# Kernel tuning notes

Hardware: AMD Instinct MI355X
Metric: run time of the kernel (lower is better)

Reference implementation:

```python
import jax, jax.numpy as jnp
import numpy as np

L, C, H, DH, M, NP, HID, NCLS, EPS = 12, 768, 12, 64, 64, 197, 3072, 1000, 1e-6

def layer_norm(x, w, b):
    mu = x.mean(-1, keepdims=True)
    var = ((x - mu) ** 2).mean(-1, keepdims=True)
    return (x - mu) * jax.lax.rsqrt(var + EPS) * w + b

def softmax_kernel(data, w, is_query):
    # data: (B,N,H,dh), w: (m,dh). Faithful to source: projection uses raw data
    # (no normalizer), and diag term is sum(data)/2 * d^{-1/2} (as written).
    d = data.shape[-1]
    dn = 1.0 / np.sqrt(np.sqrt(d))
    ratio = 1.0 / np.sqrt(np.sqrt(M))
    dd = jnp.einsum('blhd,md->blhm', data, w)
    diag = (data.sum(-1) / 2.0) * dn * dn  # (B,N,H)
    diag = diag[..., None]
    if is_query:
        stab = jnp.max(dd, axis=-1, keepdims=True)
    else:
        stab = jnp.max(dd)
    return ratio * (jnp.exp(dd - diag - stab) + 1e-6)

def performer_attn(x, qkv_w, qkv_b, w_orf, proj_w, proj_b):
    B, N, _ = x.shape
    qkv = (x @ qkv_w.T + qkv_b).reshape(B, N, 3, H, DH)
    q, k, v = qkv[:, :, 0], qkv[:, :, 1], qkv[:, :, 2]  # (B,N,H,dh)
    kp = softmax_kernel(k, w_orf, False)
    qp = softmax_kernel(q, w_orf, True)
    kv = jnp.einsum('blhm,blhd->bhmd', kp, v)
    num = jnp.einsum('blhm,bhmd->blhd', qp, kv)
    ks = kp.sum(1)  # (B,H,m)
    D = jnp.einsum('blhm,bhm->blh', qp, ks)[..., None]
    out = (num / D).reshape(B, N, C)
    return out @ proj_w.T + proj_b

def setup_inputs() -> dict:
    rng = np.random.default_rng(0)
    def rn(*s, scale=0.02):
        return jnp.asarray(rng.standard_normal(s, dtype=np.float32) * scale)
    # Gaussian orthogonal random features per layer (m == head_dim -> one QR block)
    w_orf = []
    for _ in range(L):
        blk = rng.standard_normal((DH, DH)).astype(np.float32)
        q, _ = np.linalg.qr(blk)
        mult = np.linalg.norm(rng.standard_normal((M, DH)).astype(np.float32), axis=1)
        w_orf.append(np.diag(mult) @ q.T)
    inp = {
        'x': jnp.asarray(rng.standard_normal((32, 3, 224, 224), dtype=np.float32)),
        'patch_w': rn(C, 3, 16, 16), 'patch_b': rn(C),
        'cls_token': rn(1, 1, C), 'pos_embed': rn(1, NP, C),
        'ln1_w': jnp.ones((L, C), jnp.float32), 'ln1_b': jnp.zeros((L, C), jnp.float32),
        'qkv_w': rn(L, 3 * C, C), 'qkv_b': jnp.zeros((L, 3 * C), jnp.float32),
        'w_orf': jnp.asarray(np.stack(w_orf)),
        'proj_w': rn(L, C, C), 'proj_b': jnp.zeros((L, C), jnp.float32),
        'ln2_w': jnp.ones((L, C), jnp.float32), 'ln2_b': jnp.zeros((L, C), jnp.float32),
        'fc1_w': rn(L, HID, C), 'fc1_b': jnp.zeros((L, HID), jnp.float32),
        'fc2_w': rn(L, C, HID), 'fc2_b': jnp.zeros((L, C), jnp.float32),
        'lnf_w': jnp.ones((C,), jnp.float32), 'lnf_b': jnp.zeros((C,), jnp.float32),
        'head_w': rn(NCLS, C), 'head_b': jnp.zeros((NCLS,), jnp.float32),
    }
    return inp

def reference(x, patch_w, patch_b, cls_token, pos_embed, ln1_w, ln1_b, qkv_w, qkv_b,
              w_orf, proj_w, proj_b, ln2_w, ln2_b, fc1_w, fc1_b, fc2_w, fc2_b,
              lnf_w, lnf_b, head_w, head_b):
    B = x.shape[0]
    # patch embed: 16x16 stride-16 conv -> (B, 196, 768)
    t = jax.lax.conv_general_dilated(x, patch_w, (16, 16), 'VALID',
                                     dimension_numbers=('NCHW', 'OIHW', 'NCHW'))
    t = t.reshape(B, C, -1).transpose(0, 2, 1) + patch_b
    t = jnp.concatenate([jnp.broadcast_to(cls_token, (B, 1, C)), t], axis=1) + pos_embed
    for i in range(L):
        t = t + performer_attn(layer_norm(t, ln1_w[i], ln1_b[i]),
                               qkv_w[i], qkv_b[i], w_orf[i], proj_w[i], proj_b[i])
        h = layer_norm(t, ln2_w[i], ln2_b[i])
        h = jax.nn.gelu(h @ fc1_w[i].T + fc1_b[i], approximate=False)
        t = t + (h @ fc2_w[i].T + fc2_b[i])
    t = layer_norm(t, lnf_w, lnf_b)
    return t[:, 0] @ head_w.T + head_b
```

## Files before the change

kernel.cpp:

```cpp
#include <hip/hip_runtime.h>
#include <hip/hip_bf16.h>
#include <math.h>

typedef __hip_bfloat16 bf16;

#define B_    32
#define L_    12
#define C_    768
#define H_    12
#define DH_   64
#define M_    64
#define NP_   197
#define HID_  3072
#define NCLS_ 1000
#define NTOK   (B_*NP_)
#define NPATCH (B_*196)

typedef unsigned long long u64;

__device__ __forceinline__ float ldin(const void* p, int isb, u64 i){
  return isb ? __bfloat162float(((const bf16*)p)[i]) : ((const float*)p)[i];
}

__device__ __forceinline__ unsigned short f2b(float f){
  unsigned u = __float_as_uint(f);
  u += 0x7FFFu + ((u >> 16) & 1u);
  return (unsigned short)(u >> 16);
}

__device__ __forceinline__ unsigned fkey(float f){
  unsigned u = __float_as_uint(f);
  return (u & 0x80000000u) ? ~u : (u | 0x80000000u);
}
__device__ __forceinline__ float kfloat(unsigned k){
  return __uint_as_float((k & 0x80000000u) ? (k ^ 0x80000000u) : ~k);
}

__global__ void k_detect(const void* ln1w, int* flag){
  if (threadIdx.x==0 && blockIdx.x==0)
    *flag = (((const unsigned*)ln1w)[0] == 0x3F800000u) ? 0 : 1;
}

__global__ void k_init(unsigned* Smax){
  if (threadIdx.x < L_) Smax[threadIdx.x] = 0u;
}

__global__ void k_im2col(const void* __restrict__ x, float* __restrict__ P,
                         const int* __restrict__ flag){
  int isb = *flag;
  int idx = blockIdx.x*256 + threadIdx.x;
  if (idx >= NPATCH*768) return;
  int row = idx / 768, col = idx - row*768;
  int b = row / 196, p = row - b*196;
  int py = p / 14, px = p - py*14;
  int i = col >> 8, r = col & 255, ky = r >> 4, kx = r & 15;
  P[idx] = ldin(x, isb, ((u64)(b*3+i)*224 + py*16+ky)*224 + px*16 + kx);
}

__global__ void k_assemble(const float* __restrict__ PG, const void* __restrict__ patch_b,
                           const void* __restrict__ cls, const void* __restrict__ pos,
                           float* __restrict__ T, const int* __restrict__ flag){
  int isb = *flag;
  int idx = blockIdx.x*256 + threadIdx.x;
  if (idx >= NTOK*C_) return;
  int c = idx % C_; int t = idx / C_; int n = t % NP_; int b = t / NP_;
  float v;
  if (n == 0) v = ldin(cls, isb, c) + ldin(pos, isb, c);
  else v = PG[(u64)(b*196 + n-1)*C_ + c] + ldin(patch_b, isb, c)
         + ldin(pos, isb, (u64)n*C_ + c);
  T[idx] = v;
}

__global__ void k_ln(const float* __restrict__ X, const void* __restrict__ w,
                     const void* __restrict__ bb, float* __restrict__ Y, int rowStride,
                     const int* __restrict__ flag, u64 wOff){
  int isb = *flag;
  int r = blockIdx.x;
  const float* xr = X + (u64)r*rowStride*C_;
  float* yr = Y + (u64)r*C_;
  int tid = threadIdx.x;
  int lane = tid & 63, wv = tid >> 6;
  __shared__ float red[8];
  float v[3]; float s = 0.f;
  #pragma unroll
  for (int j=0;j<3;j++){ v[j] = xr[tid + j*256]; s += v[j]; }
  #pragma unroll
  for (int off=32; off; off>>=1) s += __shfl_xor(s, off);
  if (lane==0) red[wv] = s;
  __syncthreads();
  float mu = (red[0]+red[1]+red[2]+red[3]) * (1.0f/768.0f);
  float s2 = 0.f;
  #pragma unroll
  for (int j=0;j<3;j++){ float d = v[j]-mu; s2 += d*d; }
  #pragma unroll
  for (int off=32; off; off>>=1) s2 += __shfl_xor(s2, off);
  if (lane==0) red[4+wv] = s2;
  __syncthreads();
  float rs = rsqrtf((red[4]+red[5]+red[6]+red[7])*(1.0f/768.0f) + 1e-6f);
  #pragma unroll
  for (int j=0;j<3;j++){ int c = tid + j*256;
    yr[c] = (v[j]-mu)*rs*ldin(w,isb,wOff+c) + ldin(bb,isb,wOff+c); }
}

enum {EPI_STORE=0, EPI_GELU=1, EPI_RES=2, EPI_OUT=3};

typedef __attribute__((ext_vector_type(8))) __bf16 bf16x8;
typedef __attribute__((ext_vector_type(4))) float  f32x4;

#define LDP 40

__global__ __launch_bounds__(256, 2) void k_gemm(const float* __restrict__ A,
        const void* __restrict__ W, const void* __restrict__ bias,
        float* __restrict__ D, void* __restrict__ Oany, const int* __restrict__ flag,
        int Rows, int N, int K, int epi, u64 wOff, u64 bOff){
  const int isb = *flag;
  __shared__ __bf16 Ah[128][LDP];
  __shared__ __bf16 Al[128][LDP];
  __shared__ __bf16 Bs[128][LDP];
  const int tid = threadIdx.x;
  const int rb = blockIdx.y*128, cb = blockIdx.x*128;
  const int lane = tid & 63, wv = tid >> 6;
  const int wr = (wv >> 1)*64, wc = (wv & 1)*64;
  const int lr = lane & 15, kb = (lane >> 4)*8;
  const int er = tid >> 2, kq = (tid & 3)*8;
  f32x4 acc[4][4] = {};

  for (int k0 = 0; k0 < K; k0 += 32){
    #pragma unroll
    for (int p = 0; p < 2; ++p){
      int r = er + p*64;
      int row = rb + r;
      float fv[8];
      if (row < Rows){
        const float* ap = A + (u64)row*K + k0 + kq;
        float4 f0 = *(const float4*)ap;
        float4 f1 = *(const float4*)(ap+4);
        fv[0]=f0.x; fv[1]=f0.y; fv[2]=f0.z; fv[3]=f0.w;
        fv[4]=f1.x; fv[5]=f1.y; fv[6]=f1.z; fv[7]=f1.w;
      } else {
        #pragma unroll
        for (int j=0;j<8;j++) fv[j] = 0.f;
      }
      union { uint4 v; unsigned short s[8]; } hi, lo;
      #pragma unroll
      for (int j=0;j<8;j++){
        unsigned short h = f2b(fv[j]);
        hi.s[j] = h;
        float fh = __uint_as_float((unsigned)h << 16);
        lo.s[j] = f2b(fv[j] - fh);
      }
      *(uint4*)&Ah[r][kq] = hi.v;
      *(uint4*)&Al[r][kq] = lo.v;
    }
    #pragma unroll
    for (int p = 0; p < 2; ++p){
      int r = er + p*64;
      int col = cb + r;
      union { uint4 v; unsigned short s[8]; } bw;
      if (col < N){
        if (isb){
          bw.v = *(const uint4*)((const unsigned short*)W + wOff + (u64)col*K + k0 + kq);
        } else {
          const float* wp = (const float*)W + wOff + (u64)col*K + k0 + kq;
          float4 f0 = *(const float4*)wp;
          float4 f1 = *(const float4*)(wp+4);
          bw.s[0]=f2b(f0.x); bw.s[1]=f2b(f0.y); bw.s[2]=f2b(f0.z); bw.s[3]=f2b(f0.w);
          bw.s[4]=f2b(f1.x); bw.s[5]=f2b(f1.y); bw.s[6]=f2b(f1.z); bw.s[7]=f2b(f1.w);
        }
      } else {
        bw.v = make_uint4(0u,0u,0u,0u);
      }
      *(uint4*)&Bs[r][kq] = bw.v;
    }
    __syncthreads();
    bf16x8 ah[4], al[4], bv[4];
    #pragma unroll
    for (int m=0;m<4;m++){
      ah[m] = *(const bf16x8*)&Ah[wr + m*16 + lr][kb];
      al[m] = *(const bf16x8*)&Al[wr + m*16 + lr][kb];
    }
    #pragma unroll
    for (int n=0;n<4;n++) bv[n] = *(const bf16x8*)&Bs[wc + n*16 + lr][kb];
    #pragma unroll
    for (int m=0;m<4;m++)
      #pragma unroll
      for (int n=0;n<4;n++){
        acc[m][n] = __builtin_amdgcn_mfma_f32_16x16x32_bf16(ah[m], bv[n], acc[m][n], 0, 0, 0);
        acc[m][n] = __builtin_amdgcn_mfma_f32_16x16x32_bf16(al[m], bv[n], acc[m][n], 0, 0, 0);
      }
    __syncthreads();
  }

  const int r0 = (lane >> 4)*4;
  #pragma unroll
  for (int m=0;m<4;m++){
    int rowb = rb + wr + m*16 + r0;
    #pragma unroll
    for (int n=0;n<4;n++){
      int col = cb + wc + n*16 + lr;
      if (col >= N) continue;
      float bvv = bias ? ldin(bias, isb, bOff + col) : 0.f;
      #pragma unroll
      for (int r=0;r<4;r++){
        int row = rowb + r;
        if (row >= Rows) continue;
        float v = acc[m][n][r] + bvv;
        u64 off = (u64)row*N + col;
        if (epi == EPI_STORE)      D[off] = v;
        else if (epi == EPI_GELU)  D[off] = 0.5f*v*(1.0f + erff(v*0.70710678118654752f));
        else if (epi == EPI_RES)   D[off] += v;
        else {
          if (isb) ((bf16*)Oany)[off] = __float2bfloat16(v);
          else     ((float*)Oany)[off] = v;
        }
      }
    }
  }
}

__global__ __launch_bounds__(256) void k_phi(const float* __restrict__ QKV,
        const void* __restrict__ worf, float* __restrict__ QP, float* __restrict__ KP,
        unsigned* __restrict__ Smax, const int* __restrict__ flag, u64 wOff){
  const int isb = *flag;
  __shared__ float wT[64][65];
  for (int e = threadIdx.x; e < 4096; e += 256){
    int m = e >> 6, d = e & 63;
    wT[d][m] = ldin(worf, isb, wOff + e);
  }
  __syncthreads();
  const int lane = threadIdx.x & 63, wv = threadIdx.x >> 6;
  const int NRID = NTOK*H_;
  float wmax = -1e30f;
  for (int rid = blockIdx.x*4 + wv; rid < NRID; rid += gridDim.x*4){
    int h = rid % 12, bl = rid / 12;
    const float* base = QKV + (u64)bl*2304 + h*64;
    float qd = base[lane];
    float kd = base[768 + lane];
    float sq = qd, sk = kd;
    #pragma unroll
    for (int off=32; off; off>>=1){ sq += __shfl_xor(sq,off); sk += __shfl_xor(sk,off); }
    float ddq = 0.f, ddk = 0.f;
    #pragma unroll
    for (int d=0; d<64; d++){
      float w = wT[d][lane];
      ddq += __shfl(qd, d)*w;
      ddk += __shfl(kd, d)*w;
    }
    float mq = ddq, mk = ddk;
    #pragma unroll
    for (int off=32; off; off>>=1){
      mq = fmaxf(mq, __shfl_xor(mq,off));
      mk = fmaxf(mk, __shfl_xor(mk,off));
    }
    QP[(u64)rid*64 + lane] = 0.35355339059327f*(expf(ddq - sq*0.0625f - mq) + 1e-6f);
    KP[(u64)rid*64 + lane] = ddk - sk*0.0625f;
    wmax = fmaxf(wmax, mk);
  }
  if (lane == 0) atomicMax(Smax, fkey(wmax));
}

__global__ __launch_bounds__(256) void k_kv(const float* __restrict__ KP,
        const float* __restrict__ QKV, const unsigned* __restrict__ Smax,
        float* __restrict__ KV, float* __restrict__ KS){
  const int bh = blockIdx.x, b = bh/12, h = bh - (bh/12)*12;
  const float S = kfloat(*Smax);
  __shared__ float KPs[16][64];
  __shared__ float Vs[16][64];
  const int t = threadIdx.x;
  const int d = t & 63, mg = t >> 6;
  const int lr = t >> 4, c4 = (t & 15)*4;
  float acc[16] = {};
  float ksacc = 0.f;
  for (int l0 = 0; l0 < NP_; l0 += 16){
    int l = l0 + lr;
    float4 kpv = make_float4(0.f,0.f,0.f,0.f), vv = make_float4(0.f,0.f,0.f,0.f);
    if (l < NP_){
      u64 bl = (u64)(b*NP_ + l);
      float4 r = *(const float4*)(KP + (bl*12 + h)*64 + c4);
      kpv.x = 0.35355339059327f*(expf(r.x - S) + 1e-6f);
      kpv.y = 0.35355339059327f*(expf(r.y - S) + 1e-6f);
      kpv.z = 0.35355339059327f*(expf(r.z - S) + 1e-6f);
      kpv.w = 0.35355339059327f*(expf(r.w - S) + 1e-6f);
      vv = *(const float4*)(QKV + bl*2304 + 1536 + h*64 + c4);
    }
    __syncthreads();
    *(float4*)&KPs[lr][c4] = kpv;
    *(float4*)&Vs[lr][c4]  = vv;
    __syncthreads();
    #pragma unroll
    for (int lc=0; lc<16; lc++){
      float vd = Vs[lc][d];
      #pragma unroll
      for (int j=0;j<16;j++) acc[j] += KPs[lc][mg*16+j]*vd;
    }
    if (t < 64){
      #pragma unroll
      for (int lc=0; lc<16; lc++) ksacc += KPs[lc][t];
    }
  }
  float* kvb = KV + (u64)bh*4096;
  #pragma unroll
  for (int j=0;j<16;j++) kvb[(u64)(mg*16+j)*64 + d] = acc[j];
  if (t < 64) KS[(u64)bh*64 + t] = ksacc;
}

__global__ __launch_bounds__(256) void k_numd(const float* __restrict__ QP,
        const float* __restrict__ KV, const float* __restrict__ KS,
        float* __restrict__ OUT){
  const int bh = blockIdx.x, b = bh/12, h = bh - (bh/12)*12;
  __shared__ float kvs[64][64];
  __shared__ float kss[64];
  const int t = threadIdx.x;
  for (int e = t*4; e < 4096; e += 1024)
    *(float4*)&kvs[0][e] = *(const float4*)(KV + (u64)bh*4096 + e);
  if (t < 64) kss[t] = KS[(u64)bh*64 + t];
  __syncthreads();
  const int lane = t & 63, wv = t >> 6;
  for (int l = wv; l < NP_; l += 4){
    u64 rid = (u64)(b*NP_ + l)*12 + h;
    float q = QP[rid*64 + lane];
    float dp = q*kss[lane];
    #pragma unroll
    for (int off=32; off; off>>=1) dp += __shfl_xor(dp, off);
    float acc = 0.f;
    #pragma unroll
    for (int m=0;m<64;m++) acc += __shfl(q, m)*kvs[m][lane];
    OUT[(u64)(b*NP_ + l)*768 + h*64 + lane] = acc/dp;
  }
}

extern "C" void kernel_launch(void* const* d_in, const int* in_sizes, int n_in,
                              void* d_out, int out_size, void* d_ws, size_t ws_size,
                              hipStream_t stream) {
  const void* x        = d_in[0];
  const void* patch_w  = d_in[1];
  const void* patch_b  = d_in[2];
  const void* cls_tok  = d_in[3];
  const void* pos_emb  = d_in[4];
  const void* ln1_w    = d_in[5];
  const void* ln1_b    = d_in[6];
  const void* qkv_w    = d_in[7];
  const void* qkv_b    = d_in[8];
  const void* w_orf    = d_in[9];
  const void* proj_w   = d_in[10];
  const void* proj_b   = d_in[11];
  const void* ln2_w    = d_in[12];
  const void* ln2_b    = d_in[13];
  const void* fc1_w    = d_in[14];
  const void* fc1_b    = d_in[15];
  const void* fc2_w    = d_in[16];
  const void* fc2_b    = d_in[17];
  const void* lnf_w    = d_in[18];
  const void* lnf_b    = d_in[19];
  const void* head_w   = d_in[20];
  const void* head_b   = d_in[21];

  float* ws = (float*)d_ws;
  const u64 SZ_TOKC = (u64)NTOK*C_;
  const u64 SZ_BIG  = (u64)NTOK*HID_;
  const u64 SZ_PHI  = (u64)NTOK*H_*M_;
  const u64 SZ_KV   = (u64)B_*H_*M_*DH_;
  const u64 SZ_KS   = (u64)B_*H_*M_;
  const u64 SZ_RMX  = (u64)NTOK*H_;

  float* T   = ws;
  float* LNB = T   + SZ_TOKC;
  float* BIG = LNB + SZ_TOKC;
  float* QP  = BIG + SZ_BIG;
  float* KP  = QP  + SZ_PHI;
  float* KV  = KP  + SZ_PHI;
  float* KS  = KV  + SZ_KV;
  float* RMX = KS  + SZ_KS;
  float* SS  = RMX + SZ_RMX;
  unsigned* SMAX = (unsigned*)SS;
  int*   FLG = (int*)(SS + 16);
  float* CLS = SS  + 32;

  k_detect<<<1, 64, 0, stream>>>(ln1_w, FLG);
  k_init<<<1, 64, 0, stream>>>(SMAX);

  k_im2col<<<(NPATCH*768+255)/256, 256, 0, stream>>>(x, BIG, FLG);
  k_gemm<<<dim3(6,49), 256, 0, stream>>>(BIG, patch_w, nullptr, LNB, nullptr, FLG,
                                         NPATCH, 768, 768, EPI_STORE, 0, 0);
  k_assemble<<<(NTOK*C_+255)/256, 256, 0, stream>>>(LNB, patch_b, cls_tok, pos_emb, T, FLG);

  for (int i = 0; i < L_; i++){
    u64 oQW = (u64)i*2304*C_, oQB = (u64)i*2304;
    u64 oPW = (u64)i*C_*C_,   oPB = (u64)i*C_;
    u64 o1W = (u64)i*HID_*C_, o1B = (u64)i*HID_;
    u64 o2W = (u64)i*C_*HID_, o2B = (u64)i*C_;
    u64 oL  = (u64)i*C_;
    u64 oRF = (u64)i*M_*DH_;
    k_ln<<<NTOK, 256, 0, stream>>>(T, ln1_w, ln1_b, LNB, 1, FLG, oL);
    k_gemm<<<dim3(18,50), 256, 0, stream>>>(LNB, qkv_w, qkv_b, BIG, nullptr, FLG,
                                            NTOK, 2304, 768, EPI_STORE, oQW, oQB);
    k_phi<<<512, 256, 0, stream>>>(BIG, w_orf, QP, KP, SMAX+i, FLG, oRF);
    k_kv<<<B_*H_, 256, 0, stream>>>(KP, BIG, SMAX+i, KV, KS);
    k_numd<<<B_*H_, 256, 0, stream>>>(QP, KV, KS, LNB);
    k_gemm<<<dim3(6,50), 256, 0, stream>>>(LNB, proj_w, proj_b, T, nullptr, FLG,
                                           NTOK, 768, 768, EPI_RES, oPW, oPB);
    k_ln<<<NTOK, 256, 0, stream>>>(T, ln2_w, ln2_b, LNB, 1, FLG, oL);
    k_gemm<<<dim3(24,50), 256, 0, stream>>>(LNB, fc1_w, fc1_b, BIG, nullptr, FLG,
                                            NTOK, 3072, 768, EPI_GELU, o1W, o1B);
    k_gemm<<<dim3(6,50), 256, 0, stream>>>(BIG, fc2_w, fc2_b, T, nullptr, FLG,
                                           NTOK, 768, 3072, EPI_RES, o2W, o2B);
  }

  k_ln<<<B_, 256, 0, stream>>>(T, lnf_w, lnf_b, CLS, NP_, FLG, 0);
  k_gemm<<<dim3(8,1), 256, 0, stream>>>(CLS, head_w, head_b, nullptr, d_out, FLG,
                                        B_, NCLS_, 768, EPI_OUT, 0, 0);
}
```

Baseline: 11.45 ms.

## Pre-split activations into bf16 hi/lo and stream GEMM tiles via global_load_lds

Producers (im2col, layernorm, attention output, GELU epilogue) now write activations as separate bf16 high and low halves instead of fp32. The GEMM then loads A and B tiles directly into XOR-swizzled LDS with global_load_lds, using a K step of 64. Work-groups are remapped for XCD-aware, row-stripe locality, and occupancy is raised to 3 blocks per CU. This removes per-tile fp32 to bf16 splitting and the register round-trip. In exchange, rows past the end can be read out of bounds when Rows is not a multiple of 128 (the A loads are unclamped), and the workspace layout is reshuffled.

```diff
diff --git a/kernel.cpp b/kernel.cpp
--- a/kernel.cpp
+++ b/kernel.cpp
@@ -27,6 +27,9 @@
   u += 0x7FFFu + ((u >> 16) & 1u);
   return (unsigned short)(u >> 16);
 }
+__device__ __forceinline__ float b2f(unsigned short h){
+  return __uint_as_float((unsigned)h << 16);
+}
 
 __device__ __forceinline__ unsigned fkey(float f){
   unsigned u = __float_as_uint(f);
@@ -36,6 +39,12 @@
   return __uint_as_float((k & 0x80000000u) ? (k ^ 0x80000000u) : ~k);
 }
 
+__device__ __forceinline__ void gl_lds16(const void* g, void* s){
+  __builtin_amdgcn_global_load_lds((const __attribute__((address_space(1))) unsigned int*)g,
+                                   (__attribute__((address_space(3))) unsigned int*)s,
+                                   16, 0, 0);
+}
+
 __global__ void k_detect(const void* ln1w, int* flag){
   if (threadIdx.x==0 && blockIdx.x==0)
     *flag = (((const unsigned*)ln1w)[0] == 0x3F800000u) ? 0 : 1;
@@ -45,8 +54,8 @@
   if (threadIdx.x < L_) Smax[threadIdx.x] = 0u;
 }
 
-__global__ void k_im2col(const void* __restrict__ x, float* __restrict__ P,
-                         const int* __restrict__ flag){
+__global__ void k_im2col(const void* __restrict__ x, unsigned short* __restrict__ PH,
+                         unsigned short* __restrict__ PL, const int* __restrict__ flag){
   int isb = *flag;
   int idx = blockIdx.x*256 + threadIdx.x;
   if (idx >= NPATCH*768) return;
@@ -54,7 +63,9 @@
   int b = row / 196, p = row - b*196;
   int py = p / 14, px = p - py*14;
   int i = col >> 8, r = col & 255, ky = r >> 4, kx = r & 15;
-  P[idx] = ldin(x, isb, ((u64)(b*3+i)*224 + py*16+ky)*224 + px*16 + kx);
+  float v = ldin(x, isb, ((u64)(b*3+i)*224 + py*16+ky)*224 + px*16 + kx);
+  unsigned short h = f2b(v);
+  PH[idx] = h; PL[idx] = f2b(v - b2f(h));
 }
 
 __global__ void k_assemble(const float* __restrict__ PG, const void* __restrict__ patch_b,
@@ -72,12 +83,12 @@
 }
 
 __global__ void k_ln(const float* __restrict__ X, const void* __restrict__ w,
-                     const void* __restrict__ bb, float* __restrict__ Y, int rowStride,
+                     const void* __restrict__ bb, unsigned short* __restrict__ YH,
+                     unsigned short* __restrict__ YL, int rowStride,
                      const int* __restrict__ flag, u64 wOff){
   int isb = *flag;
   int r = blockIdx.x;
   const float* xr = X + (u64)r*rowStride*C_;
-  float* yr = Y + (u64)r*C_;
   int tid = threadIdx.x;
   int lane = tid & 63, wv = tid >> 6;
   __shared__ float red[8];
@@ -99,7 +110,11 @@
   float rs = rsqrtf((red[4]+red[5]+red[6]+red[7])*(1.0f/768.0f) + 1e-6f);
   #pragma unroll
   for (int j=0;j<3;j++){ int c = tid + j*256;
-    yr[c] = (v[j]-mu)*rs*ldin(w,isb,wOff+c) + ldin(bb,isb,wOff+c); }
+    float o = (v[j]-mu)*rs*ldin(w,isb,wOff+c) + ldin(bb,isb,wOff+c);
+    unsigned short h = f2b(o);
+    YH[(u64)r*C_ + c] = h;
+    YL[(u64)r*C_ + c] = f2b(o - b2f(h));
+  }
 }
 
 enum {EPI_STORE=0, EPI_GELU=1, EPI_RES=2, EPI_OUT=3};
@@ -107,87 +122,100 @@
 typedef __attribute__((ext_vector_type(8))) __bf16 bf16x8;
 typedef __attribute__((ext_vector_type(4))) float  f32x4;
 
-#define LDP 40
-
-__global__ __launch_bounds__(256, 2) void k_gemm(const float* __restrict__ A,
+__global__ __launch_bounds__(256, 3) void k_gemm(
+        const unsigned short* __restrict__ AHp, const unsigned short* __restrict__ ALp,
         const void* __restrict__ W, const void* __restrict__ bias,
-        float* __restrict__ D, void* __restrict__ Oany, const int* __restrict__ flag,
+        float* __restrict__ Df, unsigned short* __restrict__ GH, unsigned short* __restrict__ GL,
+        void* __restrict__ Oany, const int* __restrict__ flag,
         int Rows, int N, int K, int epi, u64 wOff, u64 bOff){
   const int isb = *flag;
-  __shared__ __bf16 Ah[128][LDP];
-  __shared__ __bf16 Al[128][LDP];
-  __shared__ __bf16 Bs[128][LDP];
+  __shared__ __bf16 sAh[128*64];
+  __shared__ __bf16 sAl[128*64];
+  __shared__ __bf16 sBs[128*64];
   const int tid = threadIdx.x;
-  const int rb = blockIdx.y*128, cb = blockIdx.x*128;
   const int lane = tid & 63, wv = tid >> 6;
+
+  const int nx = (N + 127) >> 7;
+  const int nwg = gridDim.x;
+  const int q = nwg >> 3, r8 = nwg & 7;
+  const int xcd = blockIdx.x & 7, sidx = blockIdx.x >> 3;
+  const int wg = (xcd < r8 ? xcd*(q+1) : r8*(q+1) + (xcd-r8)*q) + sidx;
+  const int stripe = wg / (nx*8);
+  const int within = wg - stripe*(nx*8);
+  const int bx = within >> 3, by = stripe*8 + (within & 7);
+  const int rb = by*128, cb = bx*128;
+  if (rb >= Rows) return;
+
   const int wr = (wv >> 1)*64, wc = (wv & 1)*64;
-  const int lr = lane & 15, kb = (lane >> 4)*8;
-  const int er = tid >> 2, kq = (tid & 3)*8;
+  const int lr = lane & 15;
+  const int srow = lane >> 3;
+  const int sgb  = ((lane & 7) ^ srow) * 16;
+  const int wvBase = wv * 32;
+
+  const char* Ahb = (const char*)AHp;
+  const char* Alb = (const char*)ALp;
+  const char* Wb = nullptr; const float* Wf = nullptr;
+  unsigned limB = 0;
+  if (isb){ Wb = (const char*)W + wOff*2; limB = (unsigned)((u64)N*(u64)K*2 - 16); }
+  else      Wf = (const float*)W + wOff;
+
   f32x4 acc[4][4] = {};
 
-  for (int k0 = 0; k0 < K; k0 += 32){
-    #pragma unroll
-    for (int p = 0; p < 2; ++p){
-      int r = er + p*64;
-      int row = rb + r;
-      float fv[8];
-      if (row < Rows){
-        const float* ap = A + (u64)row*K + k0 + kq;
-        float4 f0 = *(const float4*)ap;
-        float4 f1 = *(const float4*)(ap+4);
-        fv[0]=f0.x; fv[1]=f0.y; fv[2]=f0.z; fv[3]=f0.w;
-        fv[4]=f1.x; fv[5]=f1.y; fv[6]=f1.z; fv[7]=f1.w;
-      } else {
+  for (int k0 = 0; k0 < K; k0 += 64){
+    #pragma unroll
+    for (int c = 0; c < 4; ++c){
+      int row = wvBase + c*8 + srow;
+      unsigned aoff = (unsigned)((rb + row)*K + k0)*2u + sgb;
+      gl_lds16(Ahb + aoff, &sAh[(wvBase + c*8)*64]);
+      gl_lds16(Alb + aoff, &sAl[(wvBase + c*8)*64]);
+    }
+    if (isb){
+      #pragma unroll
+      for (int c = 0; c < 4; ++c){
+        int row = wvBase + c*8 + srow;
+        unsigned boff = (unsigned)((cb + row)*K + k0)*2u + sgb;
+        boff = boff < limB ? boff : limB;
+        gl_lds16(Wb + boff, &sBs[(wvBase + c*8)*64]);
+      }
+    } else {
+      for (int e = tid; e < 1024; e += 256){
+        int rr = e >> 3, lg = e & 7;
+        int col = cb + rr;
+        union { uint4 v; unsigned short s[8]; } bw;
+        if (col < N){
+          const float* wp = Wf + (u64)col*K + k0 + lg*8;
+          #pragma unroll
+          for (int j=0;j<8;j++) bw.s[j] = f2b(wp[j]);
+        } else bw.v = make_uint4(0u,0u,0u,0u);
+        *(uint4*)&sBs[rr*64 + (lg ^ (rr & 7))*8] = bw.v;
+      }
+    }
+    __syncthreads();
+    #pragma unroll
+    for (int ks = 0; ks < 2; ++ks){
+      const int g = ks*4 + (lane >> 4);
+      bf16x8 ah[4], al[4], bv[4];
+      #pragma unroll
+      for (int m=0;m<4;m++){
+        int R = wr + m*16 + lr;
+        int gp = (g ^ (R & 7)) * 8;
+        ah[m] = *(const bf16x8*)&sAh[R*64 + gp];
+        al[m] = *(const bf16x8*)&sAl[R*64 + gp];
+      }
+      #pragma unroll
+      for (int n=0;n<4;n++){
+        int R = wc + n*16 + lr;
+        int gp = (g ^ (R & 7)) * 8;
+        bv[n] = *(const bf16x8*)&sBs[R*64 + gp];
+      }
+      #pragma unroll
+      for (int m=0;m<4;m++)
         #pragma unroll
-        for (int j=0;j<8;j++) fv[j] = 0.f;
-      }
-      union { uint4 v; unsigned short s[8]; } hi, lo;
-      #pragma unroll
-      for (int j=0;j<8;j++){
-        unsigned short h = f2b(fv[j]);
-        hi.s[j] = h;
-        float fh = __uint_as_float((unsigned)h << 16);
-        lo.s[j] = f2b(fv[j] - fh);
-      }
-      *(uint4*)&Ah[r][kq] = hi.v;
-      *(uint4*)&Al[r][kq] = lo.v;
-    }
-    #pragma unroll
-    for (int p = 0; p < 2; ++p){
-      int r = er + p*64;
-      int col = cb + r;
-      union { uint4 v; unsigned short s[8]; } bw;
-      if (col < N){
-        if (isb){
-          bw.v = *(const uint4*)((const unsigned short*)W + wOff + (u64)col*K + k0 + kq);
-        } else {
-          const float* wp = (const float*)W + wOff + (u64)col*K + k0 + kq;
-          float4 f0 = *(const float4*)wp;
-          float4 f1 = *(const float4*)(wp+4);
-          bw.s[0]=f2b(f0.x); bw.s[1]=f2b(f0.y); bw.s[2]=f2b(f0.z); bw.s[3]=f2b(f0.w);
-          bw.s[4]=f2b(f1.x); bw.s[5]=f2b(f1.y); bw.s[6]=f2b(f1.z); bw.s[7]=f2b(f1.w);
+        for (int n=0;n<4;n++){
+          acc[m][n] = __builtin_amdgcn_mfma_f32_16x16x32_bf16(ah[m], bv[n], acc[m][n], 0, 0, 0);
+          acc[m][n] = __builtin_amdgcn_mfma_f32_16x16x32_bf16(al[m], bv[n], acc[m][n], 0, 0, 0);
         }
-      } else {
-        bw.v = make_uint4(0u,0u,0u,0u);
-      }
-      *(uint4*)&Bs[r][kq] = bw.v;
-    }
-    __syncthreads();
-    bf16x8 ah[4], al[4], bv[4];
-    #pragma unroll
-    for (int m=0;m<4;m++){
-      ah[m] = *(const bf16x8*)&Ah[wr + m*16 + lr][kb];
-      al[m] = *(const bf16x8*)&Al[wr + m*16 + lr][kb];
-    }
-    #pragma unroll
-    for (int n=0;n<4;n++) bv[n] = *(const bf16x8*)&Bs[wc + n*16 + lr][kb];
-    #pragma unroll
-    for (int m=0;m<4;m++)
-      #pragma unroll
-      for (int n=0;n<4;n++){
-        acc[m][n] = __builtin_amdgcn_mfma_f32_16x16x32_bf16(ah[m], bv[n], acc[m][n], 0, 0, 0);
-        acc[m][n] = __builtin_amdgcn_mfma_f32_16x16x32_bf16(al[m], bv[n], acc[m][n], 0, 0, 0);
-      }
+    }
     __syncthreads();
   }
 
@@ -206,9 +234,13 @@
         if (row >= Rows) continue;
         float v = acc[m][n][r] + bvv;
         u64 off = (u64)row*N + col;
-        if (epi == EPI_STORE)      D[off] = v;
-        else if (epi == EPI_GELU)  D[off] = 0.5f*v*(1.0f + erff(v*0.70710678118654752f));
-        else if (epi == EPI_RES)   D[off] += v;
+        if (epi == EPI_STORE)      Df[off] = v;
+        else if (epi == EPI_GELU){
+          float gv = 0.5f*v*(1.0f + erff(v*0.70710678118654752f));
+          unsigned short h = f2b(gv);
+          GH[off] = h; GL[off] = f2b(gv - b2f(h));
+        }
+        else if (epi == EPI_RES)   Df[off] += v;
         else {
           if (isb) ((bf16*)Oany)[off] = __float2bfloat16(v);
           else     ((float*)Oany)[off] = v;
@@ -306,7 +338,7 @@
 
 __global__ __launch_bounds__(256) void k_numd(const float* __restrict__ QP,
         const float* __restrict__ KV, const float* __restrict__ KS,
-        float* __restrict__ OUT){
+        unsigned short* __restrict__ OH, unsigned short* __restrict__ OL){
   const int bh = blockIdx.x, b = bh/12, h = bh - (bh/12)*12;
   __shared__ float kvs[64][64];
   __shared__ float kss[64];
@@ -318,15 +350,24 @@
   const int lane = t & 63, wv = t >> 6;
   for (int l = wv; l < NP_; l += 4){
     u64 rid = (u64)(b*NP_ + l)*12 + h;
-    float q = QP[rid*64 + lane];
-    float dp = q*kss[lane];
+    float qv = QP[rid*64 + lane];
+    float dp = qv*kss[lane];
     #pragma unroll
     for (int off=32; off; off>>=1) dp += __shfl_xor(dp, off);
     float acc = 0.f;
     #pragma unroll
-    for (int m=0;m<64;m++) acc += __shfl(q, m)*kvs[m][lane];
-    OUT[(u64)(b*NP_ + l)*768 + h*64 + lane] = acc/dp;
-  }
+    for (int m=0;m<64;m++) acc += __shfl(qv, m)*kvs[m][lane];
+    float o = acc/dp;
+    u64 off = (u64)(b*NP_ + l)*768 + h*64 + lane;
+    unsigned short hb = f2b(o);
+    OH[off] = hb; OL[off] = f2b(o - b2f(hb));
+  }
+}
+
+static inline dim3 gemmGrid(int Rows, int N){
+  int nx = (N + 127)/128, ny = (Rows + 127)/128;
+  int nyp = ((ny + 7)/8)*8;
+  return dim3(nx*nyp);
 }
 
 extern "C" void kernel_launch(void* const* d_in, const int* in_sizes, int n_in,
@@ -357,32 +398,35 @@
 
   float* ws = (float*)d_ws;
   const u64 SZ_TOKC = (u64)NTOK*C_;
-  const u64 SZ_BIG  = (u64)NTOK*HID_;
+  const u64 SZ_A1   = (u64)NTOK*C_/2;
+  const u64 SZ_BIGR = (u64)NTOK*HID_;
   const u64 SZ_PHI  = (u64)NTOK*H_*M_;
   const u64 SZ_KV   = (u64)B_*H_*M_*DH_;
   const u64 SZ_KS   = (u64)B_*H_*M_;
-  const u64 SZ_RMX  = (u64)NTOK*H_;
-
-  float* T   = ws;
-  float* LNB = T   + SZ_TOKC;
-  float* BIG = LNB + SZ_TOKC;
-  float* QP  = BIG + SZ_BIG;
+
+  float* T    = ws;
+  float* A1f  = T + SZ_TOKC;
+  unsigned short* A1H = (unsigned short*)A1f;
+  unsigned short* A1L = A1H + (u64)NTOK*C_;
+  float* BIGR = A1f + 2*SZ_A1;
+  float* BIG  = BIGR;
+  unsigned short* A2H = (unsigned short*)BIGR;
+  unsigned short* A2L = A2H + (u64)NTOK*HID_;
+  float* QP  = BIGR + SZ_BIGR;
   float* KP  = QP  + SZ_PHI;
   float* KV  = KP  + SZ_PHI;
   float* KS  = KV  + SZ_KV;
-  float* RMX = KS  + SZ_KS;
-  float* SS  = RMX + SZ_RMX;
+  float* SS  = KS  + SZ_KS;
   unsigned* SMAX = (unsigned*)SS;
   int*   FLG = (int*)(SS + 16);
-  float* CLS = SS  + 32;
 
   k_detect<<<1, 64, 0, stream>>>(ln1_w, FLG);
   k_init<<<1, 64, 0, stream>>>(SMAX);
 
-  k_im2col<<<(NPATCH*768+255)/256, 256, 0, stream>>>(x, BIG, FLG);
-  k_gemm<<<dim3(6,49), 256, 0, stream>>>(BIG, patch_w, nullptr, LNB, nullptr, FLG,
-                                         NPATCH, 768, 768, EPI_STORE, 0, 0);
-  k_assemble<<<(NTOK*C_+255)/256, 256, 0, stream>>>(LNB, patch_b, cls_tok, pos_emb, T, FLG);
+  k_im2col<<<(NPATCH*768+255)/256, 256, 0, stream>>>(x, A1H, A1L, FLG);
+  k_gemm<<<gemmGrid(NPATCH,768), 256, 0, stream>>>(A1H, A1L, patch_w, nullptr,
+        BIG, nullptr, nullptr, nullptr, FLG, NPATCH, 768, 768, EPI_STORE, 0, 0);
+  k_assemble<<<(NTOK*C_+255)/256, 256, 0, stream>>>(BIG, patch_b, cls_tok, pos_emb, T, FLG);
 
   for (int i = 0; i < L_; i++){
     u64 oQW = (u64)i*2304*C_, oQB = (u64)i*2304;
@@ -391,22 +435,22 @@
     u64 o2W = (u64)i*C_*HID_, o2B = (u64)i*C_;
     u64 oL  = (u64)i*C_;
     u64 oRF = (u64)i*M_*DH_;
-    k_ln<<<NTOK, 256, 0, stream>>>(T, ln1_w, ln1_b, LNB, 1, FLG, oL);
-    k_gemm<<<dim3(18,50), 256, 0, stream>>>(LNB, qkv_w, qkv_b, BIG, nullptr, FLG,
-                                            NTOK, 2304, 768, EPI_STORE, oQW, oQB);
+    k_ln<<<NTOK, 256, 0, stream>>>(T, ln1_w, ln1_b, A1H, A1L, 1, FLG, oL);
+    k_gemm<<<gemmGrid(NTOK,2304), 256, 0, stream>>>(A1H, A1L, qkv_w, qkv_b,
+          BIG, nullptr, nullptr, nullptr, FLG, NTOK, 2304, 768, EPI_STORE, oQW, oQB);
     k_phi<<<512, 256, 0, stream>>>(BIG, w_orf, QP, KP, SMAX+i, FLG, oRF);
     k_kv<<<B_*H_, 256, 0, stream>>>(KP, BIG, SMAX+i, KV, KS);
-    k_numd<<<B_*H_, 256, 0, stream>>>(QP, KV, KS, LNB);
-    k_gemm<<<dim3(6,50), 256, 0, stream>>>(LNB, proj_w, proj_b, T, nullptr, FLG,
-                                           NTOK, 768, 768, EPI_RES, oPW, oPB);
-    k_ln<<<NTOK, 256, 0, stream>>>(T, ln2_w, ln2_b, LNB, 1, FLG, oL);
-    k_gemm<<<dim3(24,50), 256, 0, stream>>>(LNB, fc1_w, fc1_b, BIG, nullptr, FLG,
-                                            NTOK, 3072, 768, EPI_GELU, o1W, o1B);
-    k_gemm<<<dim3(6,50), 256, 0, stream>>>(BIG, fc2_w, fc2_b, T, nullptr, FLG,
-                                           NTOK, 768, 3072, EPI_RES, o2W, o2B);
-  }
-
-  k_ln<<<B_, 256, 0, stream>>>(T, lnf_w, lnf_b, CLS, NP_, FLG, 0);
-  k_gemm<<<dim3(8,1), 256, 0, stream>>>(CLS, head_w, head_b, nullptr, d_out, FLG,
-                                        B_, NCLS_, 768, EPI_OUT, 0, 0);
-}
+    k_numd<<<B_*H_, 256, 0, stream>>>(QP, KV, KS, A1H, A1L);
+    k_gemm<<<gemmGrid(NTOK,768), 256, 0, stream>>>(A1H, A1L, proj_w, proj_b,
+          T, nullptr, nullptr, nullptr, FLG, NTOK, 768, 768, EPI_RES, oPW, oPB);
+    k_ln<<<NTOK, 256, 0, stream>>>(T, ln2_w, ln2_b, A1H, A1L, 1, FLG, oL);
+    k_gemm<<<gemmGrid(NTOK,3072), 256, 0, stream>>>(A1H, A1L, fc1_w, fc1_b,
+          nullptr, A2H, A2L, nullptr, FLG, NTOK, 3072, 768, EPI_GELU, o1W, o1B);
+    k_gemm<<<gemmGrid(NTOK,768), 256, 0, stream>>>(A2H, A2L, fc2_w, fc2_b,
+          T, nullptr, nullptr, nullptr, FLG, NTOK, 768, 3072, EPI_RES, o2W, o2B);
+  }
+
+  k_ln<<<B_, 256, 0, stream>>>(T, lnf_w, lnf_b, A1H, A1L, NP_, FLG, 0);
+  k_gemm<<<gemmGrid(B_,NCLS_), 256, 0, stream>>>(A1H, A1L, head_w, head_b,
+        nullptr, nullptr, nullptr, d_out, FLG, B_, NCLS_, 768, EPI_OUT, 0, 0);
+}
```

Measured after the change: 10.11 ms. 11.7% less time.
